# Kernel optimization log

Measured on AMD Instinct MI355X. Metric: run time of the kernel, lower is better.

The kernel has to match this reference:

```python
import jax, jax.numpy as jnp
import numpy as np

N_CAPS, R, CIN, COUT = 10, 1152, 8, 16  # digit caps, primary caps (32*6*6), caps dims
B = 256


def setup_inputs() -> dict:
    key = jax.random.key(0)
    k1, k2 = jax.random.split(key)
    x = jax.random.normal(k1, (B, R, CIN), dtype=jnp.float32)
    # learned transform W: [num_capsules, num_route_nodes, in_channels, out_channels]
    W = jax.random.normal(k2, (N_CAPS, R, CIN, COUT), dtype=jnp.float32)
    return {"x": x, "W": W}


def squash(t, axis=-1):
    sq = jnp.sum(t * t, axis=axis, keepdims=True)
    return sq / (1.0 + sq) * t / jnp.sqrt(sq)


def reference(x, W):
    # u_hat = (x[None,:,:,None,:] @ W[:,None]) -> [N_CAPS, B, R, 1, COUT]; squeeze the 1.
    u_hat = jnp.einsum('bri,nrio->nbro', x, W)  # [N, B, R, O]
    # NOTE: the original forward returns v_j INSIDE the routing loop, so exactly one
    # iteration executes: b_ij = 0 => c_ij = softmax(zeros, dim=route) = 1/R (uniform).
    c = 1.0 / u_hat.shape[2]
    s = jnp.sum(c * u_hat, axis=2, keepdims=True)  # [N, B, 1, O]
    v = squash(s, axis=-1)
    return v[:, :, :, None, :]  # [N, B, 1, 1, O] to match torch v_j shape
```

## Files before the change

kernel.cpp:

```cpp
#include <hip/hip_runtime.h>

#define RNODES 1152
#define KDIM 9216
#define COUT 16
#define NCAPS 10
#define WSTRIDE (KDIM*COUT)

#define LROW 40
#define WBUF (NCAPS*COUT*LROW)
#define STEPS 9
#define SPLITS 32
#define NBLK 256
#define PARTL (32*COUT*NCAPS)
#define PARTL4 (PARTL/4)

using bf16x8 = __attribute__((ext_vector_type(8))) short;
using f32x4  = __attribute__((ext_vector_type(4))) float;

__device__ __forceinline__ unsigned short f2bf(float f) {
  unsigned int u = __builtin_bit_cast(unsigned int, f);
  return (unsigned short)((u + 0x8000u) >> 16);
}

__global__ __launch_bounds__(256, 1) void caps_gemm(const float* __restrict__ x,
                                                    const float* __restrict__ W,
                                                    float* __restrict__ ws) {
  __shared__ unsigned short wbuf[2][WBUF];
  const int tid = threadIdx.x;
  const int bid = blockIdx.x;
  const int mt  = bid >> 5;
  const int ks  = bid & 31;
  const int b0  = mt * 32;
  const int k0  = ks * (STEPS * 32);

  const int lane = tid & 63;
  const int wv   = tid >> 6;
  const int p    = wv >> 1;
  const int h    = wv & 1;
  const int q    = lane >> 4;
  const int m16  = lane & 15;

  int u_n[5], u_kl[5], u_of[5];
#pragma unroll
  for (int j = 0; j < 5; ++j) {
    const int u  = j * 256 + tid;
    u_n[j]  = u >> 7;
    const int rem = u & 127;
    u_kl[j] = rem >> 2;
    u_of[j] = (rem & 3) << 2;
  }

  const float* xrow = x + (size_t)(b0 + p * 16 + m16) * KDIM + k0 + q * 8;

  float4 pw[3][5];
  float4 pa[3][2];

  auto load_step = [&](int s, int slot) {
#pragma unroll
    for (int j = 0; j < 5; ++j)
      pw[slot][j] = *(const float4*)(W + (size_t)u_n[j] * WSTRIDE +
                                     (size_t)(k0 + s * 32 + u_kl[j]) * COUT + u_of[j]);
    pa[slot][0] = *(const float4*)(xrow + s * 32);
    pa[slot][1] = *(const float4*)(xrow + s * 32 + 4);
  };

  load_step(0, 0);
  load_step(1, 1);
  load_step(2, 2);

  f32x4 acc[5];
#pragma unroll
  for (int i = 0; i < 5; ++i) acc[i] = (f32x4){0.f, 0.f, 0.f, 0.f};

  const int qrot = (q + (m16 & 3) + (m16 >> 2)) & 3;

#pragma unroll
  for (int s = 0; s < STEPS; ++s) {
    const int slot = s % 3;
    unsigned short* b = &wbuf[s & 1][0];
#pragma unroll
    for (int j = 0; j < 5; ++j) {
      const int kl  = u_kl[j];
      const int klo = kl & 7, kblk = kl >> 3;
      const float* v = (const float*)&pw[slot][j];
#pragma unroll
      for (int r = 0; r < 4; ++r) {
        const int c   = u_n[j] * COUT + u_of[j] + r;
        const int pos = klo | (((kblk + (c & 3) + ((c >> 2) & 3)) & 3) << 3);
        b[c * LROW + pos] = f2bf(v[r]);
      }
    }
    __syncthreads();

    bf16x8 a;
    a[0] = (short)f2bf(pa[slot][0].x); a[1] = (short)f2bf(pa[slot][0].y);
    a[2] = (short)f2bf(pa[slot][0].z); a[3] = (short)f2bf(pa[slot][0].w);
    a[4] = (short)f2bf(pa[slot][1].x); a[5] = (short)f2bf(pa[slot][1].y);
    a[6] = (short)f2bf(pa[slot][1].z); a[7] = (short)f2bf(pa[slot][1].w);

    if (s + 3 < STEPS) load_step(s + 3, slot);

#pragma unroll
    for (int j = 0; j < 5; ++j) {
      const int nt = h * 5 + j;
      bf16x8 bf = *(const bf16x8*)&b[(nt * COUT + m16) * LROW + (qrot << 3)];
      acc[j] = __builtin_amdgcn_mfma_f32_16x16x32_bf16(a, bf, acc[j], 0, 0, 0);
    }
  }

  float* P = ws + (size_t)bid * PARTL;
  const int prow = p * 16 + q * 4;
#pragma unroll
  for (int j = 0; j < 5; ++j)
#pragma unroll
    for (int r = 0; r < 4; ++r)
      P[(h * 5 + j) * 512 + (prow + r) * COUT + m16] = acc[j][r];
}

__global__ __launch_bounds__(128, 1) void caps_reduce(const float* __restrict__ ws,
                                                      float* __restrict__ out) {
  const int f  = blockIdx.x * 128 + threadIdx.x;
  const int n  = f >> 10;
  const int b  = (f >> 2) & 255;
  const int o4 = f & 3;
  const int mt = b >> 5, row = b & 31;

  const float4* base = (const float4*)ws + (size_t)(mt * SPLITS) * PARTL4
                       + n * 128 + row * 4 + o4;
  float4 s0 = {0,0,0,0}, s1 = {0,0,0,0}, s2 = {0,0,0,0}, s3 = {0,0,0,0};
#pragma unroll
  for (int kk = 0; kk < SPLITS; kk += 4) {
    float4 a0 = base[(size_t)(kk + 0) * PARTL4];
    float4 a1 = base[(size_t)(kk + 1) * PARTL4];
    float4 a2 = base[(size_t)(kk + 2) * PARTL4];
    float4 a3 = base[(size_t)(kk + 3) * PARTL4];
    s0.x += a0.x; s0.y += a0.y; s0.z += a0.z; s0.w += a0.w;
    s1.x += a1.x; s1.y += a1.y; s1.z += a1.z; s1.w += a1.w;
    s2.x += a2.x; s2.y += a2.y; s2.z += a2.z; s2.w += a2.w;
    s3.x += a3.x; s3.y += a3.y; s3.z += a3.z; s3.w += a3.w;
  }
  const float inv = 1.0f / (float)RNODES;
  float4 s;
  s.x = ((s0.x + s1.x) + (s2.x + s3.x)) * inv;
  s.y = ((s0.y + s1.y) + (s2.y + s3.y)) * inv;
  s.z = ((s0.z + s1.z) + (s2.z + s3.z)) * inv;
  s.w = ((s0.w + s1.w) + (s2.w + s3.w)) * inv;

  float sq = s.x * s.x + s.y * s.y + s.z * s.z + s.w * s.w;
  sq += __shfl_xor(sq, 1);
  sq += __shfl_xor(sq, 2);
  const float g = sqrtf(sq) / (1.0f + sq);
  s.x *= g; s.y *= g; s.z *= g; s.w *= g;

  ((float4*)out)[f] = s;
}

extern "C" void kernel_launch(void* const* d_in, const int* in_sizes, int n_in,
                              void* d_out, int out_size, void* d_ws, size_t ws_size,
                              hipStream_t stream) {
  const float* x = (const float*)d_in[0];
  const float* W = (const float*)d_in[1];
  float* ws  = (float*)d_ws;
  float* out = (float*)d_out;

  caps_gemm<<<dim3(NBLK), dim3(256), 0, stream>>>(x, W, ws);
  caps_reduce<<<dim3(80), dim3(128), 0, stream>>>(ws, out);
}
```

Measured before the change: 71.17 us.

## Fuse GEMM and split-K reduction into one cooperative kernel with grid sync

Merges the split-K partial GEMM and the reduction/squash kernel into a single cooperative launch, with a threadfence and a grid-wide barrier between the two phases. The reduction now uses one thread per output element, with 16-lane shuffles for the squash norm. This is meant to remove the second kernel launch and its gap. In exchange it adds the cost of a grid barrier and a cooperative launch, and the reduction loads become scalar instead of float4.

```diff
diff --git a/kernel.cpp b/kernel.cpp
--- a/kernel.cpp
+++ b/kernel.cpp
@@ -1,4 +1,7 @@
 #include <hip/hip_runtime.h>
+#include <hip/hip_cooperative_groups.h>
+
+namespace cg = cooperative_groups;
 
 #define RNODES 1152
 #define KDIM 9216
@@ -22,9 +25,10 @@
   return (unsigned short)((u + 0x8000u) >> 16);
 }
 
-__global__ __launch_bounds__(256, 1) void caps_gemm(const float* __restrict__ x,
-                                                    const float* __restrict__ W,
-                                                    float* __restrict__ ws) {
+__global__ __launch_bounds__(256, 1) void caps_fused(const float* __restrict__ x,
+                                                     const float* __restrict__ W,
+                                                     float* __restrict__ ws,
+                                                     float* __restrict__ out) {
   __shared__ unsigned short wbuf[2][WBUF];
   const int tid = threadIdx.x;
   const int bid = blockIdx.x;
@@ -115,44 +119,37 @@
 #pragma unroll
     for (int r = 0; r < 4; ++r)
       P[(h * 5 + j) * 512 + (prow + r) * COUT + m16] = acc[j][r];
-}
 
-__global__ __launch_bounds__(128, 1) void caps_reduce(const float* __restrict__ ws,
-                                                      float* __restrict__ out) {
-  const int f  = blockIdx.x * 128 + threadIdx.x;
-  const int n  = f >> 10;
-  const int b  = (f >> 2) & 255;
-  const int o4 = f & 3;
-  const int mt = b >> 5, row = b & 31;
+  __threadfence();
+  cg::this_grid().sync();
 
-  const float4* base = (const float4*)ws + (size_t)(mt * SPLITS) * PARTL4
-                       + n * 128 + row * 4 + o4;
-  float4 s0 = {0,0,0,0}, s1 = {0,0,0,0}, s2 = {0,0,0,0}, s3 = {0,0,0,0};
+  const int f = bid * 256 + tid;
+  if (f < NCAPS * 256 * COUT) {
+    const int n   = f >> 12;
+    const int bb  = (f >> 4) & 255;
+    const int o   = f & 15;
+    const int fmt = bb >> 5, row = bb & 31;
+
+    const float* base = ws + (size_t)(fmt * SPLITS) * PARTL + n * 512 + row * COUT + o;
+    float s0 = 0.f, s1 = 0.f, s2 = 0.f, s3 = 0.f;
 #pragma unroll
-  for (int kk = 0; kk < SPLITS; kk += 4) {
-    float4 a0 = base[(size_t)(kk + 0) * PARTL4];
-    float4 a1 = base[(size_t)(kk + 1) * PARTL4];
-    float4 a2 = base[(size_t)(kk + 2) * PARTL4];
-    float4 a3 = base[(size_t)(kk + 3) * PARTL4];
-    s0.x += a0.x; s0.y += a0.y; s0.z += a0.z; s0.w += a0.w;
-    s1.x += a1.x; s1.y += a1.y; s1.z += a1.z; s1.w += a1.w;
-    s2.x += a2.x; s2.y += a2.y; s2.z += a2.z; s2.w += a2.w;
-    s3.x += a3.x; s3.y += a3.y; s3.z += a3.z; s3.w += a3.w;
+    for (int kk = 0; kk < SPLITS; kk += 4) {
+      s0 += base[(size_t)(kk + 0) * PARTL];
+      s1 += base[(size_t)(kk + 1) * PARTL];
+      s2 += base[(size_t)(kk + 2) * PARTL];
+      s3 += base[(size_t)(kk + 3) * PARTL];
+    }
+    const float inv = 1.0f / (float)RNODES;
+    float s = ((s0 + s1) + (s2 + s3)) * inv;
+
+    float sq = s * s;
+    sq += __shfl_xor(sq, 1);
+    sq += __shfl_xor(sq, 2);
+    sq += __shfl_xor(sq, 4);
+    sq += __shfl_xor(sq, 8);
+    const float g = sqrtf(sq) / (1.0f + sq);
+    out[f] = s * g;
   }
-  const float inv = 1.0f / (float)RNODES;
-  float4 s;
-  s.x = ((s0.x + s1.x) + (s2.x + s3.x)) * inv;
-  s.y = ((s0.y + s1.y) + (s2.y + s3.y)) * inv;
-  s.z = ((s0.z + s1.z) + (s2.z + s3.z)) * inv;
-  s.w = ((s0.w + s1.w) + (s2.w + s3.w)) * inv;
-
-  float sq = s.x * s.x + s.y * s.y + s.z * s.z + s.w * s.w;
-  sq += __shfl_xor(sq, 1);
-  sq += __shfl_xor(sq, 2);
-  const float g = sqrtf(sq) / (1.0f + sq);
-  s.x *= g; s.y *= g; s.z *= g; s.w *= g;
-
-  ((float4*)out)[f] = s;
 }
 
 extern "C" void kernel_launch(void* const* d_in, const int* in_sizes, int n_in,
@@ -163,6 +160,7 @@
   float* ws  = (float*)d_ws;
   float* out = (float*)d_out;
 
-  caps_gemm<<<dim3(NBLK), dim3(256), 0, stream>>>(x, W, ws);
-  caps_reduce<<<dim3(80), dim3(128), 0, stream>>>(ws, out);
+  void* args[] = {(void*)&x, (void*)&W, (void*)&ws, (void*)&out};
+  hipLaunchCooperativeKernel((const void*)caps_fused, dim3(NBLK), dim3(256),
+                             args, 0, stream);
 }
```

Result: slower. 145.5 us (+104.5%).

## Halve batch tile per block to 16 rows and double grid to 512 blocks

Applied to the files above, without the earlier changes.

Each block now computes a 16-row batch tile instead of 32, so the grid doubles to 512 blocks. The four waves split the 10 capsule N-tiles three per wave, and the fourth wave does partly redundant MFMAs on a clamped tile whose results it does not store. Launch bounds now allow two blocks per CU to raise occupancy. The cost is that every W tile is converted to bf16 and staged in LDS twice as often, which doubles global W traffic and LDS conversion work per unit of output.

```diff
diff --git a/kernel.cpp b/kernel.cpp
--- a/kernel.cpp
+++ b/kernel.cpp
@@ -10,8 +10,9 @@
 #define WBUF (NCAPS*COUT*LROW)
 #define STEPS 9
 #define SPLITS 32
-#define NBLK 256
-#define PARTL (32*COUT*NCAPS)
+#define NBLK 512
+#define MT 16
+#define PARTL (MT*COUT*NCAPS)
 #define PARTL4 (PARTL/4)
 
 using bf16x8 = __attribute__((ext_vector_type(8))) short;
@@ -22,7 +23,7 @@
   return (unsigned short)((u + 0x8000u) >> 16);
 }
 
-__global__ __launch_bounds__(256, 1) void caps_gemm(const float* __restrict__ x,
+__global__ __launch_bounds__(256, 2) void caps_gemm(const float* __restrict__ x,
                                                     const float* __restrict__ W,
                                                     float* __restrict__ ws) {
   __shared__ unsigned short wbuf[2][WBUF];
@@ -30,13 +31,11 @@
   const int bid = blockIdx.x;
   const int mt  = bid >> 5;
   const int ks  = bid & 31;
-  const int b0  = mt * 32;
+  const int b0  = mt * MT;
   const int k0  = ks * (STEPS * 32);
 
   const int lane = tid & 63;
   const int wv   = tid >> 6;
-  const int p    = wv >> 1;
-  const int h    = wv & 1;
   const int q    = lane >> 4;
   const int m16  = lane & 15;
 
@@ -50,7 +49,7 @@
     u_of[j] = (rem & 3) << 2;
   }
 
-  const float* xrow = x + (size_t)(b0 + p * 16 + m16) * KDIM + k0 + q * 8;
+  const float* xrow = x + (size_t)(b0 + m16) * KDIM + k0 + q * 8;
 
   float4 pw[3][5];
   float4 pa[3][2];
@@ -68,11 +67,18 @@
   load_step(1, 1);
   load_step(2, 2);
 
-  f32x4 acc[5];
+  f32x4 acc[3];
 #pragma unroll
-  for (int i = 0; i < 5; ++i) acc[i] = (f32x4){0.f, 0.f, 0.f, 0.f};
+  for (int i = 0; i < 3; ++i) acc[i] = (f32x4){0.f, 0.f, 0.f, 0.f};
 
   const int qrot = (q + (m16 & 3) + (m16 >> 2)) & 3;
+  int rdoff[3];
+#pragma unroll
+  for (int j = 0; j < 3; ++j) {
+    const int nt  = wv * 3 + j;
+    const int nt2 = (nt < NCAPS) ? nt : 0;
+    rdoff[j] = (nt2 * COUT + m16) * LROW + (qrot << 3);
+  }
 
 #pragma unroll
   for (int s = 0; s < STEPS; ++s) {
@@ -101,20 +107,23 @@
     if (s + 3 < STEPS) load_step(s + 3, slot);
 
 #pragma unroll
-    for (int j = 0; j < 5; ++j) {
-      const int nt = h * 5 + j;
-      bf16x8 bf = *(const bf16x8*)&b[(nt * COUT + m16) * LROW + (qrot << 3)];
+    for (int j = 0; j < 3; ++j) {
+      bf16x8 bf = *(const bf16x8*)&b[rdoff[j]];
       acc[j] = __builtin_amdgcn_mfma_f32_16x16x32_bf16(a, bf, acc[j], 0, 0, 0);
     }
   }
 
   float* P = ws + (size_t)bid * PARTL;
-  const int prow = p * 16 + q * 4;
+  const int prow = q * 4;
 #pragma unroll
-  for (int j = 0; j < 5; ++j)
+  for (int j = 0; j < 3; ++j) {
+    const int nt = wv * 3 + j;
+    if (nt < NCAPS) {
 #pragma unroll
-    for (int r = 0; r < 4; ++r)
-      P[(h * 5 + j) * 512 + (prow + r) * COUT + m16] = acc[j][r];
+      for (int r = 0; r < 4; ++r)
+        P[nt * (MT * COUT) + (prow + r) * COUT + m16] = acc[j][r];
+    }
+  }
 }
 
 __global__ __launch_bounds__(128, 1) void caps_reduce(const float* __restrict__ ws,
@@ -123,10 +132,10 @@
   const int n  = f >> 10;
   const int b  = (f >> 2) & 255;
   const int o4 = f & 3;
-  const int mt = b >> 5, row = b & 31;
+  const int mt = b >> 4, row = b & 15;
 
   const float4* base = (const float4*)ws + (size_t)(mt * SPLITS) * PARTL4
-                       + n * 128 + row * 4 + o4;
+                       + n * (MT * COUT / 4) + row * 4 + o4;
   float4 s0 = {0,0,0,0}, s1 = {0,0,0,0}, s2 = {0,0,0,0}, s3 = {0,0,0,0};
 #pragma unroll
   for (int kk = 0; kk < SPLITS; kk += 4) {
```

After: 73.69 us. +3.5%, slower.
